# Optimization experiments

Hardware: AMD Instinct MI355X
Metric: run time of the kernel (lower is better)

Reference implementation:

```python
import jax, jax.numpy as jnp
import numpy as np

N_HEAD = 8
D_IN = 128
D_KEY = 32
B = 65536
EPS = 1e-5
TEMP = float(D_KEY ** 0.5)


def _xavier(k, shape):
    fan_out, fan_in = shape
    limit = float(np.sqrt(6.0 / (fan_in + fan_out)))
    return jax.random.uniform(k, shape, jnp.float32, -limit, limit)


def setup_inputs() -> dict:
    key = jax.random.key(0)
    ks = jax.random.split(key, 6)
    return {
        "h_emb": jax.random.normal(ks[0], (B, D_IN), jnp.float32),
        "r_emb": jax.random.normal(ks[1], (B, D_IN), jnp.float32),
        "w_h": _xavier(ks[2], (N_HEAD * D_IN, D_IN)),
        "w_r": _xavier(ks[3], (N_HEAD * D_IN, D_IN)),
        "k_h": _xavier(ks[4], (D_KEY, D_IN)),
        "k_r": _xavier(ks[5], (D_KEY, D_IN)),
        "ln_gamma": jnp.ones((D_IN,), jnp.float32),
        "ln_beta": jnp.zeros((D_IN,), jnp.float32),
        "mode": 0,  # 0 == 'normal'
    }


def reference(h_emb, r_emb, w_h, w_r, k_h, k_r, ln_gamma, ln_beta, mode):
    # mode == 0 <=> 'normal': h_batch = h_emb.shape[0], r_batch = r_emb.shape[0]
    residual = h_emb                                     # [B, D]
    hb = h_emb.shape[0]
    rb = r_emb.shape[0]
    # linear projections to n_head copies: [1, B, H, D]
    h1 = (h_emb @ w_h.T).reshape(-1, hb, N_HEAD, D_IN)
    r1 = (r_emb @ w_r.T).reshape(-1, rb, N_HEAD, D_IN)
    # small key projections: [1, B, H, K]
    h1k = h1 @ k_h.T
    r1k = r1 @ k_r.T
    # tiny HxH attention per batch element: [1, B, H, H]
    xattn = jnp.einsum('gbhk,gbjk->gbhj', h1k / TEMP, r1k)
    g, b = xattn.shape[0], xattn.shape[1]
    xattn = jax.nn.softmax(xattn.reshape(g, b, N_HEAD * N_HEAD), axis=-1)
    xattn = xattn.reshape(g, b, N_HEAD, N_HEAD)
    h_x = xattn.sum(axis=-1)[..., None]                  # [1, B, H, 1]
    r_x = xattn.sum(axis=-2)[..., None]                  # [1, B, H, 1]
    # weighted combine + head-sum + residual: [1, B, D]
    t = (h1 * h_x + r1 * r_x).sum(axis=-2) + residual
    # LayerNorm (applied because norm_flag is False in the original)
    mu = t.mean(axis=-1, keepdims=True)
    var = ((t - mu) ** 2).mean(axis=-1, keepdims=True)
    return ln_gamma * (t - mu) / jnp.sqrt(var + EPS) + ln_beta
```

## Files before the change

kernel.cpp:

```cpp
#include <hip/hip_runtime.h>
#include <hip/hip_fp16.h>

#define NB    65536
#define DIN   128
#define TEMP_INV 0.17677669529663687f

typedef _Float16 f16x8 __attribute__((ext_vector_type(8)));
typedef float    f32x4 __attribute__((ext_vector_type(4)));

__device__ __forceinline__ ushort f2h(float x){
  __half h = __float2half(x);
  return __half_as_ushort(h);
}
__device__ __forceinline__ ushort4 f4h(float4 v){
  ushort4 o; o.x=f2h(v.x); o.y=f2h(v.y); o.z=f2h(v.z); o.w=f2h(v.w); return o;
}

__global__ void conv_w_kernel(const float* __restrict__ wh,
                              const float* __restrict__ wr,
                              ushort* __restrict__ w16h,
                              ushort* __restrict__ w16r){
  int t = blockIdx.x * 256 + threadIdx.x;
  int R  = t >> 5;
  int c4 = t & 31;
  int h  = R >> 7, np = R & 127;
  int kq = c4 >> 1, pos = (c4 & 1) * 4;
  int dst = ((h*16 + kq)*128 + np)*8 + pos;
  float4 a = ((const float4*)wh)[t];
  *(ushort4*)&w16h[dst] = f4h(a);
  float4 b = ((const float4*)wr)[t];
  *(ushort4*)&w16r[dst] = f4h(b);
}

__global__ void make_cw_kernel(const float* __restrict__ wh, const float* __restrict__ wr,
                               const float* __restrict__ kh, const float* __restrict__ kr,
                               ushort* __restrict__ cwh, ushort* __restrict__ cwr){
  int m  = blockIdx.x >> 5;
  int h  = (blockIdx.x >> 2) & 7;
  int iq = blockIdx.x & 3;
  const float* w = m ? wr : wh;
  const float* k = m ? kr : kh;
  ushort* cw = m ? cwr : cwh;

  extern __shared__ char smem[];
  float* w_s = (float*)smem;
  float* k_s = w_s + 128*32;
  int t = threadIdx.x;

  #pragma unroll
  for (int p=0;p<4;p++){
    int f = t + p*256;
    int d = f >> 3, c4 = f & 7;
    *(float4*)&w_s[d*32 + c4*4] =
        *(const float4*)&w[(size_t)(h*128 + d)*128 + iq*32 + c4*4];
  }
  #pragma unroll
  for (int p=0;p<4;p++){
    int f = t + p*256;
    ((float4*)k_s)[f] = ((const float4*)k)[f];
  }
  __syncthreads();

  int il  = t & 31;
  int kk0 = t >> 5;
  float acc[4] = {0.f,0.f,0.f,0.f};
  for (int d=0; d<128; d++){
    float wv = w_s[d*32 + il];
    #pragma unroll
    for (int j=0;j<4;j++) acc[j] += k_s[(kk0 + 8*j)*128 + d] * wv;
  }
  int i = iq*32 + il;
  #pragma unroll
  for (int j=0;j<4;j++){
    int n = h*32 + kk0 + 8*j;
    cw[(size_t)((i>>3)*256 + n)*8 + (i&7)] = f2h(acc[j]);
  }
}

__global__ __launch_bounds__(256) void attn_kernel(
    const float* __restrict__ h_emb, const float* __restrict__ r_emb,
    const ushort* __restrict__ cwh, const ushort* __restrict__ cwr,
    float* __restrict__ hx, float* __restrict__ rx){
  extern __shared__ char smem[];
  ushort* xh   = (ushort*)smem;
  ushort* xr   = xh + 4096;
  ushort* cwcH = xr + 4096;
  ushort* cwcR = cwcH + 8192;
  float*  hk   = (float*)(smem + 49152);
  float*  rk   = hk + 32*292;

  int t  = threadIdx.x;
  int b0 = blockIdx.x * 32;

  {
    const float4* gh = (const float4*)h_emb + (size_t)b0*32;
    const float4* gr = (const float4*)r_emb + (size_t)b0*32;
    #pragma unroll
    for (int p=0;p<4;p++){
      int f = t + p*256;
      int row = f >> 5, c4 = f & 31;
      int kq = c4 >> 1, pos = (c4 & 1)*4;
      *(ushort4*)&xh[(kq*32 + row)*8 + pos] = f4h(gh[f]);
      *(ushort4*)&xr[(kq*32 + row)*8 + pos] = f4h(gr[f]);
    }
  }

  int l = t & 63, w = t >> 6;
  int g = l >> 4, c = l & 15;

  f32x4 aH[2][4] = {};
  f32x4 aR[2][4] = {};

  for (int kc=0; kc<4; kc++){
    __syncthreads();
    {
      const ushort4* sH = (const ushort4*)(cwh + (size_t)kc*8192);
      const ushort4* sR = (const ushort4*)(cwr + (size_t)kc*8192);
      #pragma unroll
      for (int p=0;p<8;p++){
        int f = t + p*256;
        *(ushort4*)&cwcH[f*4] = sH[f];
        *(ushort4*)&cwcR[f*4] = sR[f];
      }
    }
    __syncthreads();
    int kqg = kc*4 + g;
    f16x8 ah0 = *(const f16x8*)&xh[(kqg*32 +      c)*8];
    f16x8 ah1 = *(const f16x8*)&xh[(kqg*32 + 16 + c)*8];
    f16x8 ar0 = *(const f16x8*)&xr[(kqg*32 +      c)*8];
    f16x8 ar1 = *(const f16x8*)&xr[(kqg*32 + 16 + c)*8];
    #pragma unroll
    for (int nt=0; nt<4; nt++){
      int n = w*64 + nt*16 + c;
      f16x8 bh = *(const f16x8*)&cwcH[(g*256 + n)*8];
      aH[0][nt] = __builtin_amdgcn_mfma_f32_16x16x32_f16(ah0, bh, aH[0][nt], 0,0,0);
      aH[1][nt] = __builtin_amdgcn_mfma_f32_16x16x32_f16(ah1, bh, aH[1][nt], 0,0,0);
      f16x8 br = *(const f16x8*)&cwcR[(g*256 + n)*8];
      aR[0][nt] = __builtin_amdgcn_mfma_f32_16x16x32_f16(ar0, br, aR[0][nt], 0,0,0);
      aR[1][nt] = __builtin_amdgcn_mfma_f32_16x16x32_f16(ar1, br, aR[1][nt], 0,0,0);
    }
  }

  #pragma unroll
  for (int mt=0; mt<2; mt++)
    #pragma unroll
    for (int nt=0; nt<4; nt++){
      int n  = w*64 + nt*16 + c;
      int hh = n >> 5, kk = n & 31;
      #pragma unroll
      for (int reg=0; reg<4; reg++){
        int e = mt*16 + g*4 + reg;
        hk[e*292 + hh*36 + kk] = aH[mt][nt][reg];
        rk[e*292 + hh*36 + kk] = aR[mt][nt][reg];
      }
    }
  __syncthreads();

  int e = t >> 3, hr = t & 7;
  const float* hkr = &hk[e*292 + hr*36];
  float4 hv[8];
  #pragma unroll
  for (int q=0;q<8;q++) hv[q] = *(const float4*)&hkr[q*4];

  float lg[8];
  #pragma unroll
  for (int j=0;j<8;j++){
    const float* rkr = &rk[e*292 + j*36];
    float s = 0.f;
    #pragma unroll
    for (int q=0;q<8;q++){
      float4 rv = *(const float4*)&rkr[q*4];
      s += hv[q].x*rv.x + hv[q].y*rv.y + hv[q].z*rv.z + hv[q].w*rv.w;
    }
    lg[j] = s * TEMP_INV;
  }
  float mx = lg[0];
  #pragma unroll
  for (int j=1;j<8;j++) mx = fmaxf(mx, lg[j]);
  mx = fmaxf(mx, __shfl_xor(mx, 1));
  mx = fmaxf(mx, __shfl_xor(mx, 2));
  mx = fmaxf(mx, __shfl_xor(mx, 4));
  float p[8]; float srow = 0.f;
  #pragma unroll
  for (int j=0;j<8;j++){ p[j] = __expf(lg[j]-mx); srow += p[j]; }
  float S = srow;
  S += __shfl_xor(S, 1); S += __shfl_xor(S, 2); S += __shfl_xor(S, 4);
  float inv = 1.0f / S;
  hx[(size_t)(b0+e)*8 + hr] = srow * inv;

  #pragma unroll
  for (int j=0;j<8;j++){
    p[j] += __shfl_xor(p[j], 1);
    p[j] += __shfl_xor(p[j], 2);
    p[j] += __shfl_xor(p[j], 4);
  }
  float cs = p[0];
  #pragma unroll
  for (int j=1;j<8;j++) cs = (hr==j) ? p[j] : cs;
  rx[(size_t)(b0+e)*8 + hr] = cs * inv;
}

__global__ __launch_bounds__(256,2) void fuse_kernel(
    const float* __restrict__ h_emb, const float* __restrict__ r_emb,
    const ushort* __restrict__ w16h, const ushort* __restrict__ w16r,
    const float* __restrict__ hx, const float* __restrict__ rx,
    const float* __restrict__ gamma, const float* __restrict__ beta,
    float* __restrict__ out){
  extern __shared__ char smem[];
  ushort* xh  = (ushort*)smem;
  ushort* xr  = xh + 8192;
  ushort* whc = xr + 8192;
  ushort* wrc = whc + 8192;
  float* hxs = (float*)(smem + 65536);
  float* rxs = hxs + 512;
  float* gs  = rxs + 512;
  float* bs  = gs + 128;
  float* red = bs + 128;

  int t  = threadIdx.x;
  int b0 = blockIdx.x * 64;

  {
    const float4* gh = (const float4*)h_emb + (size_t)b0*32;
    const float4* gr = (const float4*)r_emb + (size_t)b0*32;
    #pragma unroll
    for (int p=0;p<8;p++){
      int f = t + p*256;
      int row = f >> 5, c4 = f & 31;
      int kq = c4 >> 1, pos = (c4&1)*4;
      *(ushort4*)&xh[(kq*64 + row)*8 + pos] = f4h(gh[f]);
      *(ushort4*)&xr[(kq*64 + row)*8 + pos] = f4h(gr[f]);
    }
    if (t < 128)      ((float4*)hxs)[t]     = ((const float4*)(hx + (size_t)b0*8))[t];
    else              ((float4*)rxs)[t-128] = ((const float4*)(rx + (size_t)b0*8))[t-128];
    if (t < 32)       ((float4*)gs)[t]    = ((const float4*)gamma)[t];
    else if (t < 64)  ((float4*)bs)[t-32] = ((const float4*)beta)[t-32];
  }
  __syncthreads();

  int l = t & 63, w = t >> 6;
  int g = l >> 4, c = l & 15;
  int wr_ = w & 1, wc = w >> 1;

  f16x8 ah[2][4], ar[2][4];
  #pragma unroll
  for (int mt=0; mt<2; mt++)
    #pragma unroll
    for (int ks=0; ks<4; ks++){
      int row = wr_*32 + mt*16 + c;
      ah[mt][ks] = *(const f16x8*)&xh[((ks*4+g)*64 + row)*8];
      ar[mt][ks] = *(const f16x8*)&xr[((ks*4+g)*64 + row)*8];
    }

  f32x4 tacc[2][4] = {};

  for (int h=0; h<8; h++){
    f32x4 h1[2][4] = {};
    f32x4 r1[2][4] = {};
    for (int kc=0; kc<2; kc++){
      __syncthreads();
      {
        const ushort4* sH = (const ushort4*)(w16h + (size_t)((h*16 + kc*8)*128)*8);
        const ushort4* sR = (const ushort4*)(w16r + (size_t)((h*16 + kc*8)*128)*8);
        #pragma unroll
        for (int p=0;p<8;p++){
          int f = t + p*256;
          *(ushort4*)&whc[f*4] = sH[f];
          *(ushort4*)&wrc[f*4] = sR[f];
        }
      }
      __syncthreads();
      #pragma unroll
      for (int ks2=0; ks2<2; ks2++){
        int ks = kc*2 + ks2;
        #pragma unroll
        for (int nt=0; nt<4; nt++){
          int n = wc*64 + nt*16 + c;
          f16x8 bh = *(const f16x8*)&whc[((ks2*4+g)*128 + n)*8];
          h1[0][nt] = __builtin_amdgcn_mfma_f32_16x16x32_f16(ah[0][ks], bh, h1[0][nt], 0,0,0);
          h1[1][nt] = __builtin_amdgcn_mfma_f32_16x16x32_f16(ah[1][ks], bh, h1[1][nt], 0,0,0);
          f16x8 br = *(const f16x8*)&wrc[((ks2*4+g)*128 + n)*8];
          r1[0][nt] = __builtin_amdgcn_mfma_f32_16x16x32_f16(ar[0][ks], br, r1[0][nt], 0,0,0);
          r1[1][nt] = __builtin_amdgcn_mfma_f32_16x16x32_f16(ar[1][ks], br, r1[1][nt], 0,0,0);
        }
      }
    }
    #pragma unroll
    for (int mt=0; mt<2; mt++)
      #pragma unroll
      for (int reg=0; reg<4; reg++){
        int e = wr_*32 + mt*16 + g*4 + reg;
        float hv = hxs[e*8 + h];
        float rv = rxs[e*8 + h];
        #pragma unroll
        for (int nt=0; nt<4; nt++)
          tacc[mt][nt][reg] += hv*h1[mt][nt][reg] + rv*r1[mt][nt][reg];
      }
  }

  #pragma unroll
  for (int mt=0;mt<2;mt++)
    #pragma unroll
    for (int reg=0;reg<4;reg++){
      int e = wr_*32 + mt*16 + g*4 + reg;
      const float* resid = h_emb + (size_t)(b0+e)*128 + wc*64 + c;
      #pragma unroll
      for (int nt=0;nt<4;nt++)
        tacc[mt][nt][reg] += resid[nt*16];
    }

  #pragma unroll
  for (int mt=0;mt<2;mt++)
    #pragma unroll
    for (int reg=0;reg<4;reg++){
      float a = 0.f, b2 = 0.f;
      #pragma unroll
      for (int nt=0;nt<4;nt++){ float v = tacc[mt][nt][reg]; a += v; b2 += v*v; }
      #pragma unroll
      for (int msk=1; msk<16; msk<<=1){
        a  += __shfl_xor(a, msk);
        b2 += __shfl_xor(b2, msk);
      }
      if (c == 0){
        int e = wr_*32 + mt*16 + g*4 + reg;
        red[e*4 + wc*2]     = a;
        red[e*4 + wc*2 + 1] = b2;
      }
    }
  __syncthreads();

  #pragma unroll
  for (int mt=0;mt<2;mt++)
    #pragma unroll
    for (int reg=0;reg<4;reg++){
      int e = wr_*32 + mt*16 + g*4 + reg;
      float S1 = red[e*4 + 0] + red[e*4 + 2];
      float S2 = red[e*4 + 1] + red[e*4 + 3];
      float mu  = S1 * 0.0078125f;
      float var = S2 * 0.0078125f - mu*mu;
      float rs  = rsqrtf(var + 1e-5f);
      #pragma unroll
      for (int nt=0;nt<4;nt++){
        int col = wc*64 + nt*16 + c;
        out[(size_t)(b0+e)*128 + col] = gs[col]*((tacc[mt][nt][reg]-mu)*rs) + bs[col];
      }
    }
}

extern "C" void kernel_launch(void* const* d_in, const int* in_sizes, int n_in,
                              void* d_out, int out_size, void* d_ws, size_t ws_size,
                              hipStream_t stream){
  const float* h_emb = (const float*)d_in[0];
  const float* r_emb = (const float*)d_in[1];
  const float* w_h   = (const float*)d_in[2];
  const float* w_r   = (const float*)d_in[3];
  const float* k_h   = (const float*)d_in[4];
  const float* k_r   = (const float*)d_in[5];
  const float* gamma = (const float*)d_in[6];
  const float* beta  = (const float*)d_in[7];
  float* out = (float*)d_out;

  ushort* w16h = (ushort*)d_ws;
  ushort* w16r = w16h + 131072;
  ushort* cwh  = w16r + 131072;
  ushort* cwr  = cwh + 32768;
  float*  hx   = (float*)(cwr + 32768);
  float*  rx   = hx + 524288;

  conv_w_kernel<<<128, 256, 0, stream>>>(w_h, w_r, w16h, w16r);
  make_cw_kernel<<<64, 256, 32768, stream>>>(w_h, w_r, k_h, k_r, cwh, cwr);
  attn_kernel<<<2048, 256, 123904, stream>>>(h_emb, r_emb, cwh, cwr, hx, rx);
  fuse_kernel<<<1024, 256, 71680, stream>>>(h_emb, r_emb, w16h, w16r, hx, rx,
                                            gamma, beta, out);
}
```

Before: 233.0 us.

## Fuse attention and projection-combine kernels, fold head weights into MFMA operands

Merges the attention kernel and the weighted-combine/LayerNorm kernel into one, so the per-row head weights stay in shared memory and the input rows are converted to fp16 once, directly into registers. The head weighting is moved from the fp32 accumulators onto the fp16 A operands, so the per-head projections sum straight into a single accumulator over K=1024. B operands are now read straight from global/L2 instead of being staged through LDS with barriers. The cost is fp16 rounding of the scaled inputs and more global reads of the weights per block, with 32-row blocks instead of 64.

After: 209.6 us. 10.1% less time.

```diff
diff --git a/kernel.cpp b/kernel.cpp
--- a/kernel.cpp
+++ b/kernel.cpp
@@ -1,8 +1,6 @@
 #include <hip/hip_runtime.h>
 #include <hip/hip_fp16.h>
 
-#define NB    65536
-#define DIN   128
 #define TEMP_INV 0.17677669529663687f
 
 typedef _Float16 f16x8 __attribute__((ext_vector_type(8)));
@@ -14,6 +12,18 @@
 }
 __device__ __forceinline__ ushort4 f4h(float4 v){
   ushort4 o; o.x=f2h(v.x); o.y=f2h(v.y); o.z=f2h(v.z); o.w=f2h(v.w); return o;
+}
+__device__ __forceinline__ f16x8 cvt8(float4 a, float4 b){
+  f16x8 r;
+  r[0]=(_Float16)a.x; r[1]=(_Float16)a.y; r[2]=(_Float16)a.z; r[3]=(_Float16)a.w;
+  r[4]=(_Float16)b.x; r[5]=(_Float16)b.y; r[6]=(_Float16)b.z; r[7]=(_Float16)b.w;
+  return r;
+}
+__device__ __forceinline__ f16x8 vscale(f16x8 v, _Float16 s){
+  f16x8 r;
+  #pragma unroll
+  for (int i=0;i<8;i++) r[i] = v[i]*s;
+  return r;
 }
 
 __global__ void conv_w_kernel(const float* __restrict__ wh,
@@ -77,67 +87,57 @@
   }
 }
 
-__global__ __launch_bounds__(256) void attn_kernel(
+__global__ __launch_bounds__(256,2) void xattn_fused(
     const float* __restrict__ h_emb, const float* __restrict__ r_emb,
-    const ushort* __restrict__ cwh, const ushort* __restrict__ cwr,
-    float* __restrict__ hx, float* __restrict__ rx){
+    const ushort* __restrict__ w16h, const ushort* __restrict__ w16r,
+    const ushort* __restrict__ cwh,  const ushort* __restrict__ cwr,
+    const float* __restrict__ gamma, const float* __restrict__ beta,
+    float* __restrict__ out)
+{
   extern __shared__ char smem[];
-  ushort* xh   = (ushort*)smem;
-  ushort* xr   = xh + 4096;
-  ushort* cwcH = xr + 4096;
-  ushort* cwcR = cwcH + 8192;
-  float*  hk   = (float*)(smem + 49152);
-  float*  rk   = hk + 32*292;
-
-  int t  = threadIdx.x;
-  int b0 = blockIdx.x * 32;
-
-  {
-    const float4* gh = (const float4*)h_emb + (size_t)b0*32;
-    const float4* gr = (const float4*)r_emb + (size_t)b0*32;
-    #pragma unroll
-    for (int p=0;p<4;p++){
-      int f = t + p*256;
-      int row = f >> 5, c4 = f & 31;
-      int kq = c4 >> 1, pos = (c4 & 1)*4;
-      *(ushort4*)&xh[(kq*32 + row)*8 + pos] = f4h(gh[f]);
-      *(ushort4*)&xr[(kq*32 + row)*8 + pos] = f4h(gr[f]);
-    }
-  }
-
-  int l = t & 63, w = t >> 6;
-  int g = l >> 4, c = l & 15;
+  float* hk  = (float*)smem;
+  float* rk  = hk + 32*292;
+  float* hxs = rk + 32*292;
+  float* rxs = hxs + 288;
+  float* red = rxs + 288;
+
+  const int t  = threadIdx.x;
+  const int b0 = blockIdx.x * 32;
+  const int l  = t & 63, w = t >> 6;
+  const int g  = l >> 4, c = l & 15;
+
+  f16x8 ah[2][4], ar[2][4];
+  #pragma unroll
+  for (int mt=0; mt<2; mt++){
+    const float* ph = h_emb + ((size_t)(b0 + mt*16 + c))*128 + g*8;
+    const float* pr = r_emb + ((size_t)(b0 + mt*16 + c))*128 + g*8;
+    #pragma unroll
+    for (int ks=0; ks<4; ks++){
+      float4 lo  = *(const float4*)(ph + ks*32);
+      float4 hi  = *(const float4*)(ph + ks*32 + 4);
+      ah[mt][ks] = cvt8(lo, hi);
+      float4 lo2 = *(const float4*)(pr + ks*32);
+      float4 hi2 = *(const float4*)(pr + ks*32 + 4);
+      ar[mt][ks] = cvt8(lo2, hi2);
+    }
+  }
 
   f32x4 aH[2][4] = {};
   f32x4 aR[2][4] = {};
-
-  for (int kc=0; kc<4; kc++){
-    __syncthreads();
-    {
-      const ushort4* sH = (const ushort4*)(cwh + (size_t)kc*8192);
-      const ushort4* sR = (const ushort4*)(cwr + (size_t)kc*8192);
-      #pragma unroll
-      for (int p=0;p<8;p++){
-        int f = t + p*256;
-        *(ushort4*)&cwcH[f*4] = sH[f];
-        *(ushort4*)&cwcR[f*4] = sR[f];
-      }
-    }
-    __syncthreads();
-    int kqg = kc*4 + g;
-    f16x8 ah0 = *(const f16x8*)&xh[(kqg*32 +      c)*8];
-    f16x8 ah1 = *(const f16x8*)&xh[(kqg*32 + 16 + c)*8];
-    f16x8 ar0 = *(const f16x8*)&xr[(kqg*32 +      c)*8];
-    f16x8 ar1 = *(const f16x8*)&xr[(kqg*32 + 16 + c)*8];
-    #pragma unroll
-    for (int nt=0; nt<4; nt++){
-      int n = w*64 + nt*16 + c;
-      f16x8 bh = *(const f16x8*)&cwcH[(g*256 + n)*8];
-      aH[0][nt] = __builtin_amdgcn_mfma_f32_16x16x32_f16(ah0, bh, aH[0][nt], 0,0,0);
-      aH[1][nt] = __builtin_amdgcn_mfma_f32_16x16x32_f16(ah1, bh, aH[1][nt], 0,0,0);
-      f16x8 br = *(const f16x8*)&cwcR[(g*256 + n)*8];
-      aR[0][nt] = __builtin_amdgcn_mfma_f32_16x16x32_f16(ar0, br, aR[0][nt], 0,0,0);
-      aR[1][nt] = __builtin_amdgcn_mfma_f32_16x16x32_f16(ar1, br, aR[1][nt], 0,0,0);
+  {
+    const ushort* pH = cwh + ((size_t)g*256 + w*64 + c)*8;
+    const ushort* pR = cwr + ((size_t)g*256 + w*64 + c)*8;
+    #pragma unroll
+    for (int ks=0; ks<4; ks++){
+      #pragma unroll
+      for (int nt=0; nt<4; nt++){
+        f16x8 bh = *(const f16x8*)(pH + ((size_t)ks*1024 + nt*16)*8);
+        f16x8 br = *(const f16x8*)(pR + ((size_t)ks*1024 + nt*16)*8);
+        aH[0][nt] = __builtin_amdgcn_mfma_f32_16x16x32_f16(ah[0][ks], bh, aH[0][nt],0,0,0);
+        aH[1][nt] = __builtin_amdgcn_mfma_f32_16x16x32_f16(ah[1][ks], bh, aH[1][nt],0,0,0);
+        aR[0][nt] = __builtin_amdgcn_mfma_f32_16x16x32_f16(ar[0][ks], br, aR[0][nt],0,0,0);
+        aR[1][nt] = __builtin_amdgcn_mfma_f32_16x16x32_f16(ar[1][ks], br, aR[1][nt],0,0,0);
+      }
     }
   }
 
@@ -156,194 +156,130 @@
     }
   __syncthreads();
 
-  int e = t >> 3, hr = t & 7;
-  const float* hkr = &hk[e*292 + hr*36];
-  float4 hv[8];
-  #pragma unroll
-  for (int q=0;q<8;q++) hv[q] = *(const float4*)&hkr[q*4];
-
-  float lg[8];
-  #pragma unroll
-  for (int j=0;j<8;j++){
-    const float* rkr = &rk[e*292 + j*36];
-    float s = 0.f;
-    #pragma unroll
-    for (int q=0;q<8;q++){
-      float4 rv = *(const float4*)&rkr[q*4];
-      s += hv[q].x*rv.x + hv[q].y*rv.y + hv[q].z*rv.z + hv[q].w*rv.w;
-    }
-    lg[j] = s * TEMP_INV;
-  }
-  float mx = lg[0];
-  #pragma unroll
-  for (int j=1;j<8;j++) mx = fmaxf(mx, lg[j]);
-  mx = fmaxf(mx, __shfl_xor(mx, 1));
-  mx = fmaxf(mx, __shfl_xor(mx, 2));
-  mx = fmaxf(mx, __shfl_xor(mx, 4));
-  float p[8]; float srow = 0.f;
-  #pragma unroll
-  for (int j=0;j<8;j++){ p[j] = __expf(lg[j]-mx); srow += p[j]; }
-  float S = srow;
-  S += __shfl_xor(S, 1); S += __shfl_xor(S, 2); S += __shfl_xor(S, 4);
-  float inv = 1.0f / S;
-  hx[(size_t)(b0+e)*8 + hr] = srow * inv;
-
-  #pragma unroll
-  for (int j=0;j<8;j++){
-    p[j] += __shfl_xor(p[j], 1);
-    p[j] += __shfl_xor(p[j], 2);
-    p[j] += __shfl_xor(p[j], 4);
-  }
-  float cs = p[0];
-  #pragma unroll
-  for (int j=1;j<8;j++) cs = (hr==j) ? p[j] : cs;
-  rx[(size_t)(b0+e)*8 + hr] = cs * inv;
-}
-
-__global__ __launch_bounds__(256,2) void fuse_kernel(
-    const float* __restrict__ h_emb, const float* __restrict__ r_emb,
-    const ushort* __restrict__ w16h, const ushort* __restrict__ w16r,
-    const float* __restrict__ hx, const float* __restrict__ rx,
-    const float* __restrict__ gamma, const float* __restrict__ beta,
-    float* __restrict__ out){
-  extern __shared__ char smem[];
-  ushort* xh  = (ushort*)smem;
-  ushort* xr  = xh + 8192;
-  ushort* whc = xr + 8192;
-  ushort* wrc = whc + 8192;
-  float* hxs = (float*)(smem + 65536);
-  float* rxs = hxs + 512;
-  float* gs  = rxs + 512;
-  float* bs  = gs + 128;
-  float* red = bs + 128;
-
-  int t  = threadIdx.x;
-  int b0 = blockIdx.x * 64;
-
   {
-    const float4* gh = (const float4*)h_emb + (size_t)b0*32;
-    const float4* gr = (const float4*)r_emb + (size_t)b0*32;
-    #pragma unroll
-    for (int p=0;p<8;p++){
-      int f = t + p*256;
-      int row = f >> 5, c4 = f & 31;
-      int kq = c4 >> 1, pos = (c4&1)*4;
-      *(ushort4*)&xh[(kq*64 + row)*8 + pos] = f4h(gh[f]);
-      *(ushort4*)&xr[(kq*64 + row)*8 + pos] = f4h(gr[f]);
-    }
-    if (t < 128)      ((float4*)hxs)[t]     = ((const float4*)(hx + (size_t)b0*8))[t];
-    else              ((float4*)rxs)[t-128] = ((const float4*)(rx + (size_t)b0*8))[t-128];
-    if (t < 32)       ((float4*)gs)[t]    = ((const float4*)gamma)[t];
-    else if (t < 64)  ((float4*)bs)[t-32] = ((const float4*)beta)[t-32];
+    int e = t >> 3, hr = t & 7;
+    const float* hkr = &hk[e*292 + hr*36];
+    float4 hv4[8];
+    #pragma unroll
+    for (int q=0;q<8;q++) hv4[q] = *(const float4*)&hkr[q*4];
+
+    float lg[8];
+    #pragma unroll
+    for (int j=0;j<8;j++){
+      const float* rkr = &rk[e*292 + j*36];
+      float s = 0.f;
+      #pragma unroll
+      for (int q=0;q<8;q++){
+        float4 rv = *(const float4*)&rkr[q*4];
+        s += hv4[q].x*rv.x + hv4[q].y*rv.y + hv4[q].z*rv.z + hv4[q].w*rv.w;
+      }
+      lg[j] = s * TEMP_INV;
+    }
+    float mx = lg[0];
+    #pragma unroll
+    for (int j=1;j<8;j++) mx = fmaxf(mx, lg[j]);
+    mx = fmaxf(mx, __shfl_xor(mx, 1));
+    mx = fmaxf(mx, __shfl_xor(mx, 2));
+    mx = fmaxf(mx, __shfl_xor(mx, 4));
+    float p[8]; float srow = 0.f;
+    #pragma unroll
+    for (int j=0;j<8;j++){ p[j] = __expf(lg[j]-mx); srow += p[j]; }
+    float S = srow;
+    S += __shfl_xor(S, 1); S += __shfl_xor(S, 2); S += __shfl_xor(S, 4);
+    float inv = 1.0f / S;
+    hxs[e*9 + hr] = srow * inv;
+
+    #pragma unroll
+    for (int j=0;j<8;j++){
+      p[j] += __shfl_xor(p[j], 1);
+      p[j] += __shfl_xor(p[j], 2);
+      p[j] += __shfl_xor(p[j], 4);
+    }
+    float cs = p[0];
+    #pragma unroll
+    for (int j=1;j<8;j++) cs = (hr==j) ? p[j] : cs;
+    rxs[e*9 + hr] = cs * inv;
   }
   __syncthreads();
 
-  int l = t & 63, w = t >> 6;
-  int g = l >> 4, c = l & 15;
-  int wr_ = w & 1, wc = w >> 1;
-
-  f16x8 ah[2][4], ar[2][4];
+  const int col0 = w*32;
+  f32x4 tacc[2][2] = {};
+  {
+    const ushort* bH = w16h + ((size_t)g*128 + col0 + c)*8;
+    const ushort* bR = w16r + ((size_t)g*128 + col0 + c)*8;
+    #pragma unroll
+    for (int h=0; h<8; h++){
+      _Float16 h0 = (_Float16)hxs[c*9 + h];
+      _Float16 h1 = (_Float16)hxs[(16+c)*9 + h];
+      _Float16 r0 = (_Float16)rxs[c*9 + h];
+      _Float16 r1 = (_Float16)rxs[(16+c)*9 + h];
+      #pragma unroll
+      for (int ks=0; ks<4; ks++){
+        size_t off = (size_t)(h*16 + ks*4)*128*8;
+        f16x8 a0 = vscale(ah[0][ks], h0);
+        f16x8 a1 = vscale(ah[1][ks], h1);
+        f16x8 b0v = *(const f16x8*)(bH + off);
+        f16x8 b1v = *(const f16x8*)(bH + off + 16*8);
+        tacc[0][0] = __builtin_amdgcn_mfma_f32_16x16x32_f16(a0, b0v, tacc[0][0],0,0,0);
+        tacc[1][0] = __builtin_amdgcn_mfma_f32_16x16x32_f16(a1, b0v, tacc[1][0],0,0,0);
+        tacc[0][1] = __builtin_amdgcn_mfma_f32_16x16x32_f16(a0, b1v, tacc[0][1],0,0,0);
+        tacc[1][1] = __builtin_amdgcn_mfma_f32_16x16x32_f16(a1, b1v, tacc[1][1],0,0,0);
+        f16x8 c0 = vscale(ar[0][ks], r0);
+        f16x8 c1 = vscale(ar[1][ks], r1);
+        f16x8 d0v = *(const f16x8*)(bR + off);
+        f16x8 d1v = *(const f16x8*)(bR + off + 16*8);
+        tacc[0][0] = __builtin_amdgcn_mfma_f32_16x16x32_f16(c0, d0v, tacc[0][0],0,0,0);
+        tacc[1][0] = __builtin_amdgcn_mfma_f32_16x16x32_f16(c1, d0v, tacc[1][0],0,0,0);
+        tacc[0][1] = __builtin_amdgcn_mfma_f32_16x16x32_f16(c0, d1v, tacc[0][1],0,0,0);
+        tacc[1][1] = __builtin_amdgcn_mfma_f32_16x16x32_f16(c1, d1v, tacc[1][1],0,0,0);
+      }
+    }
+  }
+
   #pragma unroll
   for (int mt=0; mt<2; mt++)
     #pragma unroll
-    for (int ks=0; ks<4; ks++){
-      int row = wr_*32 + mt*16 + c;
-      ah[mt][ks] = *(const f16x8*)&xh[((ks*4+g)*64 + row)*8];
-      ar[mt][ks] = *(const f16x8*)&xr[((ks*4+g)*64 + row)*8];
-    }
-
-  f32x4 tacc[2][4] = {};
-
-  for (int h=0; h<8; h++){
-    f32x4 h1[2][4] = {};
-    f32x4 r1[2][4] = {};
-    for (int kc=0; kc<2; kc++){
-      __syncthreads();
-      {
-        const ushort4* sH = (const ushort4*)(w16h + (size_t)((h*16 + kc*8)*128)*8);
-        const ushort4* sR = (const ushort4*)(w16r + (size_t)((h*16 + kc*8)*128)*8);
-        #pragma unroll
-        for (int p=0;p<8;p++){
-          int f = t + p*256;
-          *(ushort4*)&whc[f*4] = sH[f];
-          *(ushort4*)&wrc[f*4] = sR[f];
-        }
-      }
-      __syncthreads();
-      #pragma unroll
-      for (int ks2=0; ks2<2; ks2++){
-        int ks = kc*2 + ks2;
-        #pragma unroll
-        for (int nt=0; nt<4; nt++){
-          int n = wc*64 + nt*16 + c;
-          f16x8 bh = *(const f16x8*)&whc[((ks2*4+g)*128 + n)*8];
-          h1[0][nt] = __builtin_amdgcn_mfma_f32_16x16x32_f16(ah[0][ks], bh, h1[0][nt], 0,0,0);
-          h1[1][nt] = __builtin_amdgcn_mfma_f32_16x16x32_f16(ah[1][ks], bh, h1[1][nt], 0,0,0);
-          f16x8 br = *(const f16x8*)&wrc[((ks2*4+g)*128 + n)*8];
-          r1[0][nt] = __builtin_amdgcn_mfma_f32_16x16x32_f16(ar[0][ks], br, r1[0][nt], 0,0,0);
-          r1[1][nt] = __builtin_amdgcn_mfma_f32_16x16x32_f16(ar[1][ks], br, r1[1][nt], 0,0,0);
-        }
-      }
-    }
-    #pragma unroll
-    for (int mt=0; mt<2; mt++)
-      #pragma unroll
-      for (int reg=0; reg<4; reg++){
-        int e = wr_*32 + mt*16 + g*4 + reg;
-        float hv = hxs[e*8 + h];
-        float rv = rxs[e*8 + h];
-        #pragma unroll
-        for (int nt=0; nt<4; nt++)
-          tacc[mt][nt][reg] += hv*h1[mt][nt][reg] + rv*r1[mt][nt][reg];
-      }
-  }
-
-  #pragma unroll
-  for (int mt=0;mt<2;mt++)
-    #pragma unroll
-    for (int reg=0;reg<4;reg++){
-      int e = wr_*32 + mt*16 + g*4 + reg;
-      const float* resid = h_emb + (size_t)(b0+e)*128 + wc*64 + c;
-      #pragma unroll
-      for (int nt=0;nt<4;nt++)
-        tacc[mt][nt][reg] += resid[nt*16];
-    }
-
-  #pragma unroll
-  for (int mt=0;mt<2;mt++)
-    #pragma unroll
-    for (int reg=0;reg<4;reg++){
-      float a = 0.f, b2 = 0.f;
-      #pragma unroll
-      for (int nt=0;nt<4;nt++){ float v = tacc[mt][nt][reg]; a += v; b2 += v*v; }
-      #pragma unroll
-      for (int msk=1; msk<16; msk<<=1){
-        a  += __shfl_xor(a, msk);
-        b2 += __shfl_xor(b2, msk);
+    for (int reg=0; reg<4; reg++){
+      int row = mt*16 + g*4 + reg;
+      const float* resid = h_emb + ((size_t)(b0+row))*128 + col0 + c;
+      tacc[mt][0][reg] += resid[0];
+      tacc[mt][1][reg] += resid[16];
+    }
+
+  #pragma unroll
+  for (int mt=0; mt<2; mt++)
+    #pragma unroll
+    for (int reg=0; reg<4; reg++){
+      float v0 = tacc[mt][0][reg], v1 = tacc[mt][1][reg];
+      float a = v0 + v1, b2 = v0*v0 + v1*v1;
+      #pragma unroll
+      for (int m=1; m<16; m<<=1){
+        a  += __shfl_xor(a,  m);
+        b2 += __shfl_xor(b2, m);
       }
       if (c == 0){
-        int e = wr_*32 + mt*16 + g*4 + reg;
-        red[e*4 + wc*2]     = a;
-        red[e*4 + wc*2 + 1] = b2;
+        int row = mt*16 + g*4 + reg;
+        red[row*8 + w*2]     = a;
+        red[row*8 + w*2 + 1] = b2;
       }
     }
   __syncthreads();
 
-  #pragma unroll
-  for (int mt=0;mt<2;mt++)
-    #pragma unroll
-    for (int reg=0;reg<4;reg++){
-      int e = wr_*32 + mt*16 + g*4 + reg;
-      float S1 = red[e*4 + 0] + red[e*4 + 2];
-      float S2 = red[e*4 + 1] + red[e*4 + 3];
+  float gam0 = gamma[col0 + c],      bet0 = beta[col0 + c];
+  float gam1 = gamma[col0 + 16 + c], bet1 = beta[col0 + 16 + c];
+  #pragma unroll
+  for (int mt=0; mt<2; mt++)
+    #pragma unroll
+    for (int reg=0; reg<4; reg++){
+      int row = mt*16 + g*4 + reg;
+      float S1 = red[row*8+0] + red[row*8+2] + red[row*8+4] + red[row*8+6];
+      float S2 = red[row*8+1] + red[row*8+3] + red[row*8+5] + red[row*8+7];
       float mu  = S1 * 0.0078125f;
       float var = S2 * 0.0078125f - mu*mu;
       float rs  = rsqrtf(var + 1e-5f);
-      #pragma unroll
-      for (int nt=0;nt<4;nt++){
-        int col = wc*64 + nt*16 + c;
-        out[(size_t)(b0+e)*128 + col] = gs[col]*((tacc[mt][nt][reg]-mu)*rs) + bs[col];
-      }
+      float* po = out + ((size_t)(b0+row))*128 + col0 + c;
+      po[0]  = gam0*((tacc[mt][0][reg]-mu)*rs) + bet0;
+      po[16] = gam1*((tacc[mt][1][reg]-mu)*rs) + bet1;
     }
 }
 
@@ -364,12 +300,9 @@
   ushort* w16r = w16h + 131072;
   ushort* cwh  = w16r + 131072;
   ushort* cwr  = cwh + 32768;
-  float*  hx   = (float*)(cwr + 32768);
-  float*  rx   = hx + 524288;
 
   conv_w_kernel<<<128, 256, 0, stream>>>(w_h, w_r, w16h, w16r);
   make_cw_kernel<<<64, 256, 32768, stream>>>(w_h, w_r, k_h, k_r, cwh, cwr);
-  attn_kernel<<<2048, 256, 123904, stream>>>(h_emb, r_emb, cwh, cwr, hx, rx);
-  fuse_kernel<<<1024, 256, 71680, stream>>>(h_emb, r_emb, w16h, w16r, hx, rx,
-                                            gamma, beta, out);
-}
+  xattn_fused<<<2048, 256, 78080, stream>>>(h_emb, r_emb, w16h, w16r,
+                                            cwh, cwr, gamma, beta, out);
+}
```
